# Kernel optimization log

Hardware: AMD Instinct MI355X
Metric: run time of the kernel (lower is better)

## Reference

```python
import jax, jax.numpy as jnp
import numpy as np

H, W = 1200, 1920
B = 4
NBINS = 256
MIN_CLIP = 1.0 / ((1 << 20) - 1)
LOG_MIN_CLIP = float(np.log(MIN_CLIP))


def _mask_rows_cols():
    # Reproduces make_histo_sampling: the mask is separable (outer product of
    # a row-mask and a col-mask), so we only need the index sets.
    wb, hb = W / 42.0, H / 42.0
    xs, ys = set(), set()
    for bx in range(21):
        base = int(bx * wb)
        for tx in range(40):
            x = (tx + 5 + base) << 1  # bayer_x = 0
            if x < W:
                xs.add(x)
    for by in range(21):
        base = int(by * hb)
        for ty in range(25):
            y = (ty + 4 + base) << 1  # bayer_y = 0
            if y < H:
                ys.add(y)
    row = np.zeros(H, bool); row[sorted(ys)] = True
    col = np.zeros(W, bool); col[sorted(xs)] = True
    # crop [4:H, 4:W] then nearest-resize back to (H, W)
    row_c, col_c = row[4:H], col[4:W]
    iy = (np.arange(H) * (H - 4)) // H
    ix = (np.arange(W) * (W - 4)) // W
    rows = np.nonzero(row_c[iy])[0].astype(np.int32)
    cols = np.nonzero(col_c[ix])[0].astype(np.int32)
    return rows, cols

_ROWS, _COLS = _mask_rows_cols()


def _crop_slices():
    crops = []
    for scale in (1, 3, 7):
        for i in range(scale):
            for j in range(scale):
                x1 = int(j / scale * W); x2 = int((j + 1) / scale * W)
                y1 = int(i / scale * H); y2 = int((i + 1) / scale * H)
                x1 = x1 + x1 % 2                       # bayer_j = 0 -> even
                y1 = y1 + y1 % 2 + (1 - 2 * (y1 % 2))  # bayer_i = 1 -> odd
                crops.append((y1, y2, x1, x2))
    return crops

_CROPS = _crop_slices()  # 1 + 9 + 49 = 59 crops


def _merge_capture(img):
    s = jnp.round(img * 4095.0)
    low, mid, high = s[:, 0], s[:, 1], s[:, 2]
    low_m = jnp.where(mid == 4095.0, low, 0.0)
    high_m = jnp.where(mid <= 255.0, high, 0.0)
    mid_m = jnp.where((mid >= 256.0) & (mid <= 4094.0), mid, 0.0)
    return (high_m / 256.0 + mid_m / 16.0 + low_m)[:, None]  # (B,1,H,W)


def _hist(x):
    # x: (B, n) in [0, 1] -> torch.histc(bins=256, min=0, max=1) semantics
    b = jnp.clip((x * NBINS).astype(jnp.int32), 0, NBINS - 1)
    oh = jax.vmap(lambda bi: jnp.zeros(NBINS, jnp.float32).at[bi].add(1.0))(b)
    return oh / jnp.maximum(oh.sum(axis=1, keepdims=True), 1e-4) * NBINS


def _conv(x, w, b, stride):
    y = jax.lax.conv_general_dilated(x, w, stride, 'VALID',
                                     dimension_numbers=('NCHW', 'OIHW', 'NCHW'))
    return y + b[None, :, None, None]


def reference(img, w1, b1, w2, b2, w3, b3, w4, b4, w5, b5, w6, b6):
    m = _merge_capture(img)                                   # (B,1,H,W)
    flat = m[:, 0][:, _ROWS][:, :, _COLS].reshape(img.shape[0], -1)
    k = max(1, flat.shape[1] // 2)
    median = jnp.maximum(jnp.sort(flat, axis=1)[:, k - 1], MIN_CLIP)
    scale = (1.0 / (1024.0 * median))[:, None, None, None]
    m = jnp.minimum(m * scale, 1.0)
    m = (LOG_MIN_CLIP - jnp.log(jnp.maximum(m, MIN_CLIP))) / LOG_MIN_CLIP
    # multi-scale per-crop histograms, expo-major column order
    hists = [_hist(m[:, 0, y1:y2:2, x1:x2:2].reshape(m.shape[0], -1))
             for (y1, y2, x1, x2) in _CROPS]                  # each (B,256)
    net = jnp.stack(hists, axis=1).reshape(-1, NBINS).T[None, None]  # (1,1,256,B*59)
    net = jax.nn.relu(_conv(net, w1, b1, (4, 4)))
    net = jax.nn.relu(_conv(net, w2, b2, (4, 4)))
    net = jax.nn.relu(_conv(net, w3, b3, (4, 4)))
    net = jax.nn.relu(_conv(net, w4, b4, (4, 4)))
    net = jax.nn.relu(_conv(net, w5, b5, (1, 1)))
    out = _conv(net, w6, b6, (1, 1))                          # (1,1,1,1)
    out = (2.0 * (jax.nn.sigmoid(3.0 * out) - 0.5)).squeeze(1)
    out = out * float(np.log(4.0))
    return jnp.exp(out)                                       # (1,1,1)


def setup_inputs() -> dict:
    key = jax.random.key(0)
    ks = jax.random.split(key, 13)
    img = jax.random.uniform(ks[0], (B, 3, H, W), dtype=jnp.float32)

    def w_init(k, shape):
        fan_in = shape[1] * shape[2] * shape[3]
        return jax.random.normal(k, shape, dtype=jnp.float32) / np.sqrt(fan_in)

    nw = [128, 256, 512, 1024, 16]
    return {
        'img': img,
        'w1': w_init(ks[1], (nw[0], 1, 4, 1)),      'b1': jnp.zeros(nw[0], jnp.float32),
        'w2': w_init(ks[2], (nw[1], nw[0], 4, 1)),  'b2': jnp.zeros(nw[1], jnp.float32),
        'w3': w_init(ks[3], (nw[2], nw[1], 4, 1)),  'b3': jnp.zeros(nw[2], jnp.float32),
        'w4': w_init(ks[4], (nw[3], nw[2], 4, 1)),  'b4': jnp.zeros(nw[3], jnp.float32),
        'w5': w_init(ks[5], (nw[4], nw[3], 1, 1)),  'b5': jnp.zeros(nw[4], jnp.float32),
        'w6': w_init(ks[6], (1, nw[4], 1, 1)),      'b6': jnp.zeros(1, jnp.float32),
    }
```

## Files before the change

### kernel.cpp

```cpp
#include <hip/hip_runtime.h>

#define HH 1200
#define WW 1920
#define HW (HH*WW)
#define MINC (1.0f/1048575.0f)
#define LOGMC (-13.862942657524135f)
#define CROP_N 576000

#define O_COARSE 0
#define O_FINE   16384
#define O_HIST   17408
#define O_ROWIDX 18432
#define O_COLIDX 20864
#define O_INTS   24704
#define O_A2     24768
#define O_A3     41152
#define O_A4     49344
#define WS_TOTAL 53440
#define ZERO_BYTES 18432

__device__ __forceinline__ float merge3(float low, float mid, float high) {
    float lm = (mid == 4095.0f) ? low : 0.0f;
    float hm = (mid <= 255.0f) ? high : 0.0f;
    float mm = (mid >= 256.0f && mid <= 4094.0f) ? mid : 0.0f;
    return hm * (1.0f/256.0f) + mm * (1.0f/16.0f) + lm;
}

__device__ __forceinline__ int merged_q(const float* img, int idx) {
    float low  = rintf(img[idx] * 4095.0f);
    float mid  = rintf(img[idx + HW] * 4095.0f);
    float high = rintf(img[idx + 2*HW] * 4095.0f);
    float v = merge3(low, mid, high);
    return __float2int_rn(v * 256.0f);
}

__global__ void k_setup(int* rowidx, int* colidx, int* ints) {
    __shared__ unsigned char rmask[HH];
    __shared__ unsigned char cmask[WW];
    __shared__ int s_nr, s_nc;
    int t = threadIdx.x;
    for (int i = t; i < HH; i += 256) rmask[i] = 0;
    for (int i = t; i < WW; i += 256) cmask[i] = 0;
    if (t == 0) { s_nr = 0; s_nc = 0; }
    __syncthreads();
    for (int p = t; p < 21*25; p += 256) {
        int by = p / 25, ty = p % 25;
        int base = (int)(by * (1200.0 / 42.0));
        int y = (ty + 4 + base) << 1;
        if (y < HH) rmask[y] = 1;
    }
    for (int p = t; p < 21*40; p += 256) {
        int bx = p / 40, tx = p % 40;
        int base = (int)(bx * (1920.0 / 42.0));
        int x = (tx + 5 + base) << 1;
        if (x < WW) cmask[x] = 1;
    }
    __syncthreads();
    for (int i = t; i < HH; i += 256) {
        int iy = i * (HH - 4) / HH;
        if (rmask[iy + 4]) { int pos = atomicAdd(&s_nr, 1); rowidx[pos] = i; }
    }
    for (int i = t; i < WW; i += 256) {
        int ix = i * (WW - 4) / WW;
        if (cmask[ix + 4]) { int pos = atomicAdd(&s_nc, 1); colidx[pos] = i; }
    }
    __syncthreads();
    if (t == 0) {
        ints[3] = s_nr;
        ints[4] = s_nc;
        long long n = (long long)s_nr * (long long)s_nc;
        long long k = n >> 1;
        if (k < 1) k = 1;
        ints[0] = (int)k;
    }
}

__global__ void k_coarse(const float* __restrict__ img,
                         const int* __restrict__ rowidx,
                         const int* __restrict__ colidx,
                         const int* __restrict__ ints,
                         unsigned int* coarse) {
    __shared__ unsigned int lh[4096];
    int t = threadIdx.x;
    for (int i = t; i < 4096; i += 256) lh[i] = 0;
    __syncthreads();
    int nr = ints[3], nc = ints[4];
    int total = nr * nc;
    int stride = gridDim.x * blockDim.x;
    for (int p = blockIdx.x * 256 + t; p < total; p += stride) {
        int r = p / nc, c = p - r * nc;
        int idx = rowidx[r] * WW + colidx[c];
        int q = merged_q(img, idx);
        atomicAdd(&lh[q >> 8], 1u);
    }
    __syncthreads();
    for (int i = t; i < 4096; i += 256) {
        unsigned int v = lh[i];
        if (v) atomicAdd(&coarse[i], v);
    }
}

__global__ void k_coarsesel(const unsigned int* __restrict__ coarse, int* ints) {
    __shared__ unsigned int part[1024];
    int t = threadIdx.x;
    unsigned int b0 = coarse[t*4], b1 = coarse[t*4+1], b2 = coarse[t*4+2], b3 = coarse[t*4+3];
    unsigned int s = b0 + b1 + b2 + b3;
    part[t] = s;
    __syncthreads();
    for (int off = 1; off < 1024; off <<= 1) {
        unsigned int v = (t >= off) ? part[t - off] : 0u;
        __syncthreads();
        part[t] += v;
        __syncthreads();
    }
    unsigned int incl = part[t];
    unsigned int excl = incl - s;
    unsigned int k = (unsigned int)ints[0];
    if (excl < k && k <= incl) {
        unsigned int bs[4] = {b0, b1, b2, b3};
        unsigned int cum = excl;
        for (int i = 0; i < 4; i++) {
            if (cum + bs[i] >= k) { ints[1] = t*4 + i; ints[2] = (int)(k - cum); break; }
            cum += bs[i];
        }
    }
}

__global__ void k_fine(const float* __restrict__ img,
                       const int* __restrict__ rowidx,
                       const int* __restrict__ colidx,
                       const int* __restrict__ ints,
                       unsigned int* fine) {
    __shared__ unsigned int lh[256];
    int t = threadIdx.x;
    lh[t] = 0;
    __syncthreads();
    int nr = ints[3], nc = ints[4], T = ints[1];
    int total = nr * nc;
    int stride = gridDim.x * blockDim.x;
    for (int p = blockIdx.x * 256 + t; p < total; p += stride) {
        int r = p / nc, c = p - r * nc;
        int idx = rowidx[r] * WW + colidx[c];
        int q = merged_q(img, idx);
        if ((q >> 8) == T) atomicAdd(&lh[q & 255], 1u);
    }
    __syncthreads();
    if (lh[t]) atomicAdd(&fine[t], lh[t]);
}

#define CROP_PPT 8
__global__ void k_crophist(const float* __restrict__ img,
                           const unsigned int* __restrict__ fine,
                           const int* __restrict__ ints,
                           unsigned int* hist) {
    __shared__ unsigned int lh[256];
    __shared__ unsigned int sf[256];
    __shared__ float s_scale;
    int t = threadIdx.x;
    lh[t] = 0;
    sf[t] = fine[t];
    __syncthreads();
    if (t == 0) {
        int kprime = ints[2];
        int T = ints[1];
        unsigned int cum = 0;
        int j = 0;
        for (; j < 256; j++) { cum += sf[j]; if ((int)cum >= kprime) break; }
        if (j > 255) j = 255;
        float median = fmaxf((float)(T*256 + j) * (1.0f/256.0f), MINC);
        s_scale = 1.0f / (1024.0f * median);
    }
    __syncthreads();
    float scale = s_scale;
    int base = blockIdx.x * (256*CROP_PPT);
    for (int i = 0; i < CROP_PPT; i++) {
        int p = base + i*256 + t;
        if (p < CROP_N) {
            int pr = p / 960;
            int py = 1 + 2*pr;
            int px = 2*(p - pr*960);
            int idx = py * WW + px;
            float low  = rintf(img[idx] * 4095.0f);
            float mid  = rintf(img[idx + HW] * 4095.0f);
            float high = rintf(img[idx + 2*HW] * 4095.0f);
            float v = merge3(low, mid, high);
            float mv = fminf(v * scale, 1.0f);
            mv = fmaxf(mv, MINC);
            float tt = (LOGMC - logf(mv)) / LOGMC;
            int b = (int)(tt * 256.0f);
            if (b < 0) b = 0;
            if (b > 255) b = 255;
            atomicAdd(&lh[b], 1u);
        }
    }
    __syncthreads();
    if (lh[t]) atomicAdd(&hist[t], lh[t]);
}

__global__ void k_l12(const unsigned int* __restrict__ hist,
                      const float* __restrict__ w1, const float* __restrict__ b1,
                      const float* __restrict__ w2, const float* __restrict__ b2,
                      float* a2) {
    __shared__ float sa1[8192];
    int t = threadIdx.x;
    for (int j = t; j < 8192; j += 256) {
        int oc = j >> 6, r = j & 63;
        float acc = b1[oc];
        for (int kh = 0; kh < 4; kh++) {
            float h = ((float)hist[4*r + kh] / 576000.0f) * 256.0f;
            acc += h * w1[oc*4 + kh];
        }
        sa1[j] = fmaxf(acc, 0.0f);
    }
    __syncthreads();
    int o = blockIdx.x * 256 + t;
    int oc = o >> 4, r = o & 15;
    float acc = b2[oc];
    const float* wp = w2 + oc*128*4;
    for (int ic = 0; ic < 128; ic++) {
        const float* ap = sa1 + ic*64 + 4*r;
        acc += ap[0]*wp[ic*4+0] + ap[1]*wp[ic*4+1] + ap[2]*wp[ic*4+2] + ap[3]*wp[ic*4+3];
    }
    a2[o] = fmaxf(acc, 0.0f);
}

__global__ void k_l3(const float* __restrict__ a2, const float* __restrict__ w3,
                     const float* __restrict__ b3, float* a3) {
    __shared__ float sa2[4096];
    int t = threadIdx.x;
    int oc = blockIdx.x;
    for (int i = t; i < 4096; i += 256) sa2[i] = a2[i];
    __syncthreads();
    int r = t >> 6, lane = t & 63;
    const float* wp = w3 + oc*1024;
    float p = 0.0f;
    for (int ii = 0; ii < 4; ii++) {
        int ic = lane + 64*ii;
        const float* ap = sa2 + ic*16 + 4*r;
        const float* w = wp + ic*4;
        p += ap[0]*w[0] + ap[1]*w[1] + ap[2]*w[2] + ap[3]*w[3];
    }
    for (int off = 32; off > 0; off >>= 1) p += __shfl_down(p, off, 64);
    if (lane == 0) a3[oc*4 + r] = fmaxf(p + b3[oc], 0.0f);
}

__global__ void k_l4(const float* __restrict__ a3, const float* __restrict__ w4,
                     const float* __restrict__ b4, float* a4) {
    __shared__ float red[4];
    int t = threadIdx.x;
    int oc = blockIdx.x;
    const float* wp = w4 + oc*2048;
    float p = 0.0f;
    for (int i = 0; i < 8; i++) {
        int m = t + 256*i;
        p += a3[m] * wp[m];
    }
    for (int off = 32; off > 0; off >>= 1) p += __shfl_down(p, off, 64);
    int lane = t & 63;
    if (lane == 0) red[t >> 6] = p;
    __syncthreads();
    if (t == 0) a4[oc] = fmaxf(red[0]+red[1]+red[2]+red[3] + b4[oc], 0.0f);
}

__global__ void k_l56(const float* __restrict__ a4,
                      const float* __restrict__ w5, const float* __restrict__ b5,
                      const float* __restrict__ w6, const float* __restrict__ b6,
                      float* out) {
    __shared__ float sa5[16];
    int t = threadIdx.x;
    int w = t >> 6, lane = t & 63;
    const float* wp = w5 + w*1024;
    float p = 0.0f;
    for (int i = 0; i < 16; i++) {
        int ic = lane + 64*i;
        p += a4[ic] * wp[ic];
    }
    for (int off = 32; off > 0; off >>= 1) p += __shfl_down(p, off, 64);
    if (lane == 0) sa5[w] = fmaxf(p + b5[w], 0.0f);
    __syncthreads();
    if (t == 0) {
        float o = b6[0];
        for (int ic = 0; ic < 16; ic++) o += sa5[ic] * w6[ic];
        float s = 1.0f / (1.0f + expf(-3.0f * o));
        float y = 2.0f * (s - 0.5f) * 1.3862943611198906f;
        out[0] = expf(y);
    }
}

extern "C" void kernel_launch(void* const* d_in, const int* in_sizes, int n_in,
                              void* d_out, int out_size, void* d_ws, size_t ws_size,
                              hipStream_t stream) {
    const float* img = (const float*)d_in[0];
    const float* w1 = (const float*)d_in[1];
    const float* b1 = (const float*)d_in[2];
    const float* w2 = (const float*)d_in[3];
    const float* b2 = (const float*)d_in[4];
    const float* w3 = (const float*)d_in[5];
    const float* b3 = (const float*)d_in[6];
    const float* w4 = (const float*)d_in[7];
    const float* b4 = (const float*)d_in[8];
    const float* w5 = (const float*)d_in[9];
    const float* b5 = (const float*)d_in[10];
    const float* w6 = (const float*)d_in[11];
    const float* b6 = (const float*)d_in[12];
    float* out = (float*)d_out;

    char* ws = (char*)d_ws;
    unsigned int* coarse = (unsigned int*)(ws + O_COARSE);
    unsigned int* fine   = (unsigned int*)(ws + O_FINE);
    unsigned int* hist   = (unsigned int*)(ws + O_HIST);
    int* rowidx = (int*)(ws + O_ROWIDX);
    int* colidx = (int*)(ws + O_COLIDX);
    int* ints   = (int*)(ws + O_INTS);
    float* a2 = (float*)(ws + O_A2);
    float* a3 = (float*)(ws + O_A3);
    float* a4 = (float*)(ws + O_A4);

    hipMemsetAsync(d_ws, 0, ZERO_BYTES, stream);

    k_setup<<<1, 256, 0, stream>>>(rowidx, colidx, ints);
    k_coarse<<<256, 256, 0, stream>>>(img, rowidx, colidx, ints, coarse);
    k_coarsesel<<<1, 1024, 0, stream>>>(coarse, ints);
    k_fine<<<256, 256, 0, stream>>>(img, rowidx, colidx, ints, fine);
    k_crophist<<<(CROP_N + 256*CROP_PPT - 1)/(256*CROP_PPT), 256, 0, stream>>>(img, fine, ints, hist);
    k_l12<<<16, 256, 0, stream>>>(hist, w1, b1, w2, b2, a2);
    k_l3<<<512, 256, 0, stream>>>(a2, w3, b3, a3);
    k_l4<<<1024, 256, 0, stream>>>(a3, w4, b4, a4);
    k_l56<<<1, 1024, 0, stream>>>(a4, w5, b5, w6, b6, out);
}
```

Before: 71.19 us.

## Fuse setup and selection kernels into histogram passes, cut launch count

```diff
diff --git a/kernel.cpp b/kernel.cpp
--- a/kernel.cpp
+++ b/kernel.cpp
@@ -10,14 +10,12 @@
 #define O_COARSE 0
 #define O_FINE   16384
 #define O_HIST   17408
-#define O_ROWIDX 18432
-#define O_COLIDX 20864
-#define O_INTS   24704
-#define O_A2     24768
-#define O_A3     41152
-#define O_A4     49344
-#define WS_TOTAL 53440
-#define ZERO_BYTES 18432
+#define O_INTS   18432
+#define O_A2     18448
+#define O_A3     34832
+#define O_A4     43024
+#define WS_TOTAL 47120
+#define ZERO_U32 4612
 
 __device__ __forceinline__ float merge3(float low, float mid, float high) {
     float lm = (mid == 4095.0f) ? low : 0.0f;
@@ -26,7 +24,7 @@
     return hm * (1.0f/256.0f) + mm * (1.0f/16.0f) + lm;
 }
 
-__device__ __forceinline__ int merged_q(const float* img, int idx) {
+__device__ __forceinline__ int merged_q(const float* __restrict__ img, int idx) {
     float low  = rintf(img[idx] * 4095.0f);
     float mid  = rintf(img[idx + HW] * 4095.0f);
     float high = rintf(img[idx + 2*HW] * 4095.0f);
@@ -34,63 +32,62 @@
     return __float2int_rn(v * 256.0f);
 }
 
-__global__ void k_setup(int* rowidx, int* colidx, int* ints) {
-    __shared__ unsigned char rmask[HH];
-    __shared__ unsigned char cmask[WW];
-    __shared__ int s_nr, s_nc;
-    int t = threadIdx.x;
-    for (int i = t; i < HH; i += 256) rmask[i] = 0;
-    for (int i = t; i < WW; i += 256) cmask[i] = 0;
-    if (t == 0) { s_nr = 0; s_nc = 0; }
+__device__ __forceinline__ void build_masks(unsigned char* rawr, unsigned char* rawc,
+                                            unsigned char* colf, short* rowlist,
+                                            int* s_nr, int* s_nc) {
+    int t = threadIdx.x;
+    for (int i = t; i < HH; i += 256) rawr[i] = 0;
+    for (int i = t; i < WW; i += 256) rawc[i] = 0;
+    if (t == 0) { *s_nr = 0; *s_nc = 0; }
     __syncthreads();
     for (int p = t; p < 21*25; p += 256) {
         int by = p / 25, ty = p % 25;
         int base = (int)(by * (1200.0 / 42.0));
         int y = (ty + 4 + base) << 1;
-        if (y < HH) rmask[y] = 1;
+        if (y < HH) rawr[y] = 1;
     }
     for (int p = t; p < 21*40; p += 256) {
         int bx = p / 40, tx = p % 40;
         int base = (int)(bx * (1920.0 / 42.0));
         int x = (tx + 5 + base) << 1;
-        if (x < WW) cmask[x] = 1;
+        if (x < WW) rawc[x] = 1;
     }
     __syncthreads();
     for (int i = t; i < HH; i += 256) {
         int iy = i * (HH - 4) / HH;
-        if (rmask[iy + 4]) { int pos = atomicAdd(&s_nr, 1); rowidx[pos] = i; }
+        if (rawr[iy + 4]) { int pos = atomicAdd(s_nr, 1); rowlist[pos] = (short)i; }
     }
     for (int i = t; i < WW; i += 256) {
         int ix = i * (WW - 4) / WW;
-        if (cmask[ix + 4]) { int pos = atomicAdd(&s_nc, 1); colidx[pos] = i; }
-    }
-    __syncthreads();
-    if (t == 0) {
-        ints[3] = s_nr;
-        ints[4] = s_nc;
-        long long n = (long long)s_nr * (long long)s_nc;
-        long long k = n >> 1;
-        if (k < 1) k = 1;
-        ints[0] = (int)k;
-    }
-}
-
-__global__ void k_coarse(const float* __restrict__ img,
-                         const int* __restrict__ rowidx,
-                         const int* __restrict__ colidx,
-                         const int* __restrict__ ints,
-                         unsigned int* coarse) {
+        unsigned char v = rawc[ix + 4];
+        colf[i] = v;
+        if (v) atomicAdd(s_nc, 1);
+    }
+    __syncthreads();
+}
+
+__global__ void k_zero(unsigned int* ws) {
+    int t = threadIdx.x;
+    for (int i = t; i < ZERO_U32; i += 256) ws[i] = 0u;
+}
+
+__global__ void k_coarse(const float* __restrict__ img, unsigned int* coarse) {
+    __shared__ unsigned char rawr[HH];
+    __shared__ unsigned char rawc[WW];
+    __shared__ unsigned char colf[WW];
+    __shared__ short rowlist[HH];
+    __shared__ int s_nr, s_nc;
     __shared__ unsigned int lh[4096];
     int t = threadIdx.x;
     for (int i = t; i < 4096; i += 256) lh[i] = 0;
-    __syncthreads();
-    int nr = ints[3], nc = ints[4];
-    int total = nr * nc;
-    int stride = gridDim.x * blockDim.x;
+    build_masks(rawr, rawc, colf, rowlist, &s_nr, &s_nc);
+    int nr = s_nr;
+    int total = nr * WW;
+    int stride = gridDim.x * 256;
     for (int p = blockIdx.x * 256 + t; p < total; p += stride) {
-        int r = p / nc, c = p - r * nc;
-        int idx = rowidx[r] * WW + colidx[c];
-        int q = merged_q(img, idx);
+        int r = p / WW, c = p - r * WW;
+        if (!colf[c]) continue;
+        int q = merged_q(img, (int)rowlist[r] * WW + c);
         atomicAdd(&lh[q >> 8], 1u);
     }
     __syncthreads();
@@ -100,52 +97,59 @@
     }
 }
 
-__global__ void k_coarsesel(const unsigned int* __restrict__ coarse, int* ints) {
-    __shared__ unsigned int part[1024];
-    int t = threadIdx.x;
-    unsigned int b0 = coarse[t*4], b1 = coarse[t*4+1], b2 = coarse[t*4+2], b3 = coarse[t*4+3];
-    unsigned int s = b0 + b1 + b2 + b3;
-    part[t] = s;
-    __syncthreads();
-    for (int off = 1; off < 1024; off <<= 1) {
-        unsigned int v = (t >= off) ? part[t - off] : 0u;
+__global__ void k_fine(const float* __restrict__ img,
+                       const unsigned int* __restrict__ coarse,
+                       unsigned int* fine, int* ints) {
+    __shared__ unsigned char rawr[HH];
+    __shared__ unsigned char rawc[WW];
+    __shared__ unsigned char colf[WW];
+    __shared__ short rowlist[HH];
+    __shared__ int s_nr, s_nc;
+    __shared__ unsigned int csum[256];
+    __shared__ unsigned int lfine[256];
+    __shared__ int sT, skp;
+    int t = threadIdx.x;
+    lfine[t] = 0;
+    build_masks(rawr, rawc, colf, rowlist, &s_nr, &s_nc);
+    int nr = s_nr, nc = s_nc;
+    long long n = (long long)nr * (long long)nc;
+    unsigned int k = (unsigned int)((n >> 1) < 1 ? 1 : (n >> 1));
+
+    unsigned int mybins[16];
+    unsigned int mysum = 0;
+    #pragma unroll
+    for (int i = 0; i < 16; i++) { mybins[i] = coarse[t*16 + i]; mysum += mybins[i]; }
+    csum[t] = mysum;
+    __syncthreads();
+    for (int off = 1; off < 256; off <<= 1) {
+        unsigned int v = (t >= off) ? csum[t - off] : 0u;
         __syncthreads();
-        part[t] += v;
+        csum[t] += v;
         __syncthreads();
     }
-    unsigned int incl = part[t];
-    unsigned int excl = incl - s;
-    unsigned int k = (unsigned int)ints[0];
+    unsigned int incl = csum[t], excl = incl - mysum;
     if (excl < k && k <= incl) {
-        unsigned int bs[4] = {b0, b1, b2, b3};
         unsigned int cum = excl;
-        for (int i = 0; i < 4; i++) {
-            if (cum + bs[i] >= k) { ints[1] = t*4 + i; ints[2] = (int)(k - cum); break; }
-            cum += bs[i];
+        #pragma unroll
+        for (int i = 0; i < 16; i++) {
+            if (cum + mybins[i] >= k) { sT = t*16 + i; skp = (int)(k - cum); break; }
+            cum += mybins[i];
         }
     }
-}
-
-__global__ void k_fine(const float* __restrict__ img,
-                       const int* __restrict__ rowidx,
-                       const int* __restrict__ colidx,
-                       const int* __restrict__ ints,
-                       unsigned int* fine) {
-    __shared__ unsigned int lh[256];
-    int t = threadIdx.x;
-    lh[t] = 0;
-    __syncthreads();
-    int nr = ints[3], nc = ints[4], T = ints[1];
-    int total = nr * nc;
-    int stride = gridDim.x * blockDim.x;
+    __syncthreads();
+    int T = sT;
+    if (t == 0 && blockIdx.x == 0) { ints[0] = sT; ints[1] = skp; }
+
+    int total = nr * WW;
+    int stride = gridDim.x * 256;
     for (int p = blockIdx.x * 256 + t; p < total; p += stride) {
-        int r = p / nc, c = p - r * nc;
-        int idx = rowidx[r] * WW + colidx[c];
-        int q = merged_q(img, idx);
-        if ((q >> 8) == T) atomicAdd(&lh[q & 255], 1u);
-    }
-    __syncthreads();
-    if (lh[t]) atomicAdd(&fine[t], lh[t]);
+        int r = p / WW, c = p - r * WW;
+        if (!colf[c]) continue;
+        int q = merged_q(img, (int)rowlist[r] * WW + c);
+        if ((q >> 8) == T) atomicAdd(&lfine[q & 255], 1u);
+    }
+    __syncthreads();
+    if (lfine[t]) atomicAdd(&fine[t], lfine[t]);
 }
 
 #define CROP_PPT 8
@@ -154,20 +158,24 @@
                            const int* __restrict__ ints,
                            unsigned int* hist) {
     __shared__ unsigned int lh[256];
-    __shared__ unsigned int sf[256];
+    __shared__ unsigned int fsum[256];
     __shared__ float s_scale;
     int t = threadIdx.x;
     lh[t] = 0;
-    sf[t] = fine[t];
-    __syncthreads();
-    if (t == 0) {
-        int kprime = ints[2];
-        int T = ints[1];
-        unsigned int cum = 0;
-        int j = 0;
-        for (; j < 256; j++) { cum += sf[j]; if ((int)cum >= kprime) break; }
-        if (j > 255) j = 255;
-        float median = fmaxf((float)(T*256 + j) * (1.0f/256.0f), MINC);
+    unsigned int fv = fine[t];
+    fsum[t] = fv;
+    __syncthreads();
+    for (int off = 1; off < 256; off <<= 1) {
+        unsigned int v = (t >= off) ? fsum[t - off] : 0u;
+        __syncthreads();
+        fsum[t] += v;
+        __syncthreads();
+    }
+    unsigned int incl = fsum[t], excl = incl - fv;
+    unsigned int kp = (unsigned int)ints[1];
+    int T = ints[0];
+    if (excl < kp && kp <= incl) {
+        float median = fmaxf((float)(T*256 + t) * (1.0f/256.0f), MINC);
         s_scale = 1.0f / (1024.0f * median);
     }
     __syncthreads();
@@ -245,8 +253,13 @@
 }
 
 __global__ void k_l4(const float* __restrict__ a3, const float* __restrict__ w4,
-                     const float* __restrict__ b4, float* a4) {
+                     const float* __restrict__ b4, float* a4,
+                     const float* __restrict__ w5, const float* __restrict__ b5,
+                     const float* __restrict__ w6, const float* __restrict__ b6,
+                     int* done, float* out) {
     __shared__ float red[4];
+    __shared__ int s_last;
+    __shared__ float sa5[16];
     int t = threadIdx.x;
     int oc = blockIdx.x;
     const float* wp = w4 + oc*2048;
@@ -259,24 +272,26 @@
     int lane = t & 63;
     if (lane == 0) red[t >> 6] = p;
     __syncthreads();
-    if (t == 0) a4[oc] = fmaxf(red[0]+red[1]+red[2]+red[3] + b4[oc], 0.0f);
-}
-
-__global__ void k_l56(const float* __restrict__ a4,
-                      const float* __restrict__ w5, const float* __restrict__ b5,
-                      const float* __restrict__ w6, const float* __restrict__ b6,
-                      float* out) {
-    __shared__ float sa5[16];
-    int t = threadIdx.x;
-    int w = t >> 6, lane = t & 63;
-    const float* wp = w5 + w*1024;
-    float p = 0.0f;
-    for (int i = 0; i < 16; i++) {
-        int ic = lane + 64*i;
-        p += a4[ic] * wp[ic];
-    }
-    for (int off = 32; off > 0; off >>= 1) p += __shfl_down(p, off, 64);
-    if (lane == 0) sa5[w] = fmaxf(p + b5[w], 0.0f);
+    if (t == 0) {
+        a4[oc] = fmaxf(red[0]+red[1]+red[2]+red[3] + b4[oc], 0.0f);
+        __threadfence();
+        int v = atomicAdd(done, 1);
+        s_last = (v == (int)gridDim.x - 1) ? 1 : 0;
+    }
+    __syncthreads();
+    if (!s_last) return;
+    __threadfence();
+    int w = t >> 6;
+    for (int o = w; o < 16; o += 4) {
+        const float* wq = w5 + o*1024;
+        float q = 0.0f;
+        for (int i = 0; i < 16; i++) {
+            int ic = lane + 64*i;
+            q += a4[ic] * wq[ic];
+        }
+        for (int off = 32; off > 0; off >>= 1) q += __shfl_down(q, off, 64);
+        if (lane == 0) sa5[o] = fmaxf(q + b5[o], 0.0f);
+    }
     __syncthreads();
     if (t == 0) {
         float o = b6[0];
@@ -309,22 +324,17 @@
     unsigned int* coarse = (unsigned int*)(ws + O_COARSE);
     unsigned int* fine   = (unsigned int*)(ws + O_FINE);
     unsigned int* hist   = (unsigned int*)(ws + O_HIST);
-    int* rowidx = (int*)(ws + O_ROWIDX);
-    int* colidx = (int*)(ws + O_COLIDX);
     int* ints   = (int*)(ws + O_INTS);
     float* a2 = (float*)(ws + O_A2);
     float* a3 = (float*)(ws + O_A3);
     float* a4 = (float*)(ws + O_A4);
-
-    hipMemsetAsync(d_ws, 0, ZERO_BYTES, stream);
-
-    k_setup<<<1, 256, 0, stream>>>(rowidx, colidx, ints);
-    k_coarse<<<256, 256, 0, stream>>>(img, rowidx, colidx, ints, coarse);
-    k_coarsesel<<<1, 1024, 0, stream>>>(coarse, ints);
-    k_fine<<<256, 256, 0, stream>>>(img, rowidx, colidx, ints, fine);
+    int* done = ints + 2;
+
+    k_zero<<<1, 256, 0, stream>>>((unsigned int*)ws);
+    k_coarse<<<512, 256, 0, stream>>>(img, coarse);
+    k_fine<<<512, 256, 0, stream>>>(img, coarse, fine, ints);
     k_crophist<<<(CROP_N + 256*CROP_PPT - 1)/(256*CROP_PPT), 256, 0, stream>>>(img, fine, ints, hist);
     k_l12<<<16, 256, 0, stream>>>(hist, w1, b1, w2, b2, a2);
     k_l3<<<512, 256, 0, stream>>>(a2, w3, b3, a3);
-    k_l4<<<1024, 256, 0, stream>>>(a3, w4, b4, a4);
-    k_l56<<<1, 1024, 0, stream>>>(a4, w5, b5, w6, b6, out);
-}
+    k_l4<<<1024, 256, 0, stream>>>(a3, w4, b4, a4, w5, b5, w6, b6, done, out);
+}
```

Result: slower. 98.43 us (+38.3%).
